# Optimization experiments

Measured on AMD Instinct MI355X. Metric: run time of the kernel, lower is better.

## Reference

```python
import jax, jax.numpy as jnp
import numpy as np

B, S, L, E, H, T, V, D = 32, 256, 24, 300, 256, 16, 50000, 256  # batch, sents, words/sent, emb, gru_units, topics, vocab, dense


def setup_inputs() -> dict:
    key = jax.random.key(0)
    ks = jax.random.split(key, 12)
    word_ids = jax.random.randint(ks[0], (B, S, L), 0, V, dtype=jnp.int32)
    tsize = S // T
    starts = (jnp.arange(T, dtype=jnp.int32) * tsize + 1)          # 1-indexed inclusive
    ends = (jnp.arange(T, dtype=jnp.int32) * tsize + tsize)
    topic_start_ends = jnp.broadcast_to(jnp.stack([starts, ends], -1)[None], (B, T, 2))
    g = lambda k, shape, sc=0.05: (jax.random.normal(k, shape, jnp.float32) * sc)
    return {
        "word_ids": word_ids,
        "topic_start_ends": topic_start_ends,
        "emb": g(ks[1], (V, E), 0.1),
        "Wih_f": g(ks[2], (3 * H, E)), "Whh_f": g(ks[3], (3 * H, H)),
        "bih_f": jnp.zeros((3 * H,), jnp.float32), "bhh_f": jnp.zeros((3 * H,), jnp.float32),
        "Wih_b": g(ks[4], (3 * H, E)), "Whh_b": g(ks[5], (3 * H, H)),
        "bih_b": jnp.zeros((3 * H,), jnp.float32), "bhh_b": jnp.zeros((3 * H,), jnp.float32),
        "W_att": g(ks[6], (4 * H, 4 * H)), "v_att": g(ks[7], (4 * H, 1)),
        "W_dna": g(ks[8], (4 * H, D)), "b_dna": jnp.zeros((D,), jnp.float32),
        "W_out": g(ks[9], (D, 1)), "b_out": jnp.zeros((1,), jnp.float32),
    }


def _gru_dir(x, Wih, Whh, bih, bhh, reverse):
    # x: [B, S, E] -> outputs [B, S, H], final hidden [B, H]  (PyTorch GRU cell math)
    def step(h, xt):
        gi = xt @ Wih.T + bih
        gh = h @ Whh.T + bhh
        ir, iz, inn = jnp.split(gi, 3, axis=-1)
        hr, hz, hn = jnp.split(gh, 3, axis=-1)
        r = jax.nn.sigmoid(ir + hr)
        z = jax.nn.sigmoid(iz + hz)
        n = jnp.tanh(inn + r * hn)
        h2 = (1.0 - z) * n + z * h
        return h2, h2
    h0 = jnp.zeros((x.shape[0], Whh.shape[1]), x.dtype)
    hT, ys = jax.lax.scan(step, h0, jnp.swapaxes(x, 0, 1), reverse=reverse)
    return jnp.swapaxes(ys, 0, 1), hT


def _gather_seq(x, idx):
    # x: [B, S', C], idx: [B, K] -> [B, K, C]
    return jnp.take_along_axis(x, idx[:, :, None].astype(jnp.int32), axis=1)


def reference(word_ids, topic_start_ends, emb, Wih_f, Whh_f, bih_f, bhh_f,
              Wih_b, Whh_b, bih_b, bhh_b, W_att, v_att, W_dna, b_dna, W_out, b_out):
    # --- sent_encoder: per-sentence mean of word embeddings ---
    sent_vecs = jnp.mean(emb[word_ids], axis=2)  # [B, S, E]

    # --- doc_encoder: bidirectional GRU ---
    out_f, hT_f = _gru_dir(sent_vecs, Wih_f, Whh_f, bih_f, bhh_f, reverse=False)
    out_b, hT_b = _gru_dir(sent_vecs, Wih_b, Whh_b, bih_b, bhh_b, reverse=True)
    sent_rep = jnp.concatenate([out_f, out_b], axis=-1)          # [B, S, 2H]
    hidden = jnp.stack([hT_f, hT_b], axis=0)                     # [2, B, H]
    # faithful to torch: hidden.view(batch_size, 2H) (row-major reshape)
    doc_vec = hidden.reshape(B, 2 * H)
    doc_rep = jnp.broadcast_to(doc_vec[:, None, :], (B, S, 2 * H))

    # --- topic representation via boundary differencing on front/back-padded output ---
    padded = jnp.pad(sent_rep, ((0, 0), (1, 1), (0, 0)))         # [B, S+2, 2H]
    starts = topic_start_ends[..., 0]                            # [B, T], 1-indexed
    ends = topic_start_ends[..., 1]
    topic_fwd = _gather_seq(padded, ends)[..., :H] - _gather_seq(padded, starts - 1)[..., :H]
    topic_bwd = _gather_seq(padded, starts)[..., H:] - _gather_seq(padded, ends + 1)[..., H:]
    topic_mat = jnp.concatenate([topic_fwd, topic_bwd], axis=-1)  # [B, T, 2H]
    # sentence s (0-indexed) -> topic t with starts[t] <= s+1 <= ends[t]
    sent_1idx = jnp.arange(1, S + 1, dtype=jnp.int32)
    topic_id = jax.vmap(lambda e: jnp.searchsorted(e, sent_1idx, side='left'))(ends)  # [B, S]
    topic_rep = jnp.take_along_axis(topic_mat, topic_id[:, :, None], axis=1)          # [B, S, 2H]

    # --- decoder_attention ---
    cat_ds = jnp.concatenate([doc_rep, sent_rep], axis=-1)       # [B, S, 4H]
    cat_ts = jnp.concatenate([topic_rep, sent_rep], axis=-1)
    doc_scores = jnp.tanh(cat_ds @ W_att) @ v_att                # [B, S, 1]
    topic_scores = jnp.tanh(cat_ts @ W_att) @ v_att
    doc_w = jax.nn.softmax(doc_scores, axis=1)
    topic_w = jax.nn.softmax(topic_scores, axis=1)
    context = doc_w * doc_rep + topic_w * topic_rep              # [B, S, 2H]
    inp = jnp.concatenate([sent_rep, context], axis=-1)          # [B, S, 4H]
    h = jax.nn.relu(inp @ W_dna + b_dna)                         # dropout is identity (eval)
    logits = (h @ W_out + b_out)[..., 0]                         # [B, S]
    return logits
```

## Files before the change

kernel.cpp:

```cpp
#include <hip/hip_runtime.h>
#include <hip/hip_bf16.h>
#include <math.h>

#define Bd 32
#define Sd 256
#define Ld 24
#define Ed 300
#define Hd 256
#define Td 16
#define Dd 256
#define EP 320
#define HPAD 264

using short8 = __attribute__((ext_vector_type(8))) short;
using f32x4  = __attribute__((ext_vector_type(4))) float;

__device__ __forceinline__ float fsigm(float x) { return 1.f / (1.f + __expf(-x)); }
__device__ __forceinline__ float ftanh(float x) {
  float e = __expf(2.f * x);
  return 1.f - 2.f / (e + 1.f);
}

__global__ void sent_means_kernel(const int* __restrict__ wids,
                                  const float* __restrict__ emb,
                                  __hip_bfloat16* __restrict__ apad) {
  int r = blockIdx.x;
  __shared__ int ids[Ld];
  int tid = threadIdx.x;
  if (tid < Ld) ids[tid] = wids[r * Ld + tid];
  __syncthreads();
  float acc = 0.f;
  if (tid < Ed) {
#pragma unroll
    for (int w = 0; w < Ld; ++w) acc += emb[(size_t)ids[w] * Ed + tid];
    acc *= (1.f / 24.f);
  }
  apad[r * EP + tid] = __float2bfloat16(tid < Ed ? acc : 0.f);
}

__global__ void pad_wih_kernel(const float* __restrict__ src,
                               __hip_bfloat16* __restrict__ dst) {
  int i = blockIdx.x * 256 + threadIdx.x;
  if (i >= 768 * EP) return;
  int n = i / EP, k = i % EP;
  dst[i] = __float2bfloat16(k < Ed ? src[n * Ed + k] : 0.f);
}
__global__ void f2bf_kernel(const float* __restrict__ src,
                            __hip_bfloat16* __restrict__ dst, int n) {
  int i = blockIdx.x * 256 + threadIdx.x;
  if (i < n) dst[i] = __float2bfloat16(src[i]);
}
__global__ void transpose_att_kernel(const float* __restrict__ src,
                                     __hip_bfloat16* __restrict__ dst) {
  int i = blockIdx.x * 256 + threadIdx.x;
  int n = i >> 10, k = i & 1023;
  dst[i] = __float2bfloat16(src[k * 1024 + n]);
}
__global__ void transpose_dna_kernel(const float* __restrict__ src,
                                     __hip_bfloat16* __restrict__ dst) {
  int i = blockIdx.x * 256 + threadIdx.x;
  int n = i >> 10, k = i & 1023;
  dst[i] = __float2bfloat16(src[k * Dd + n]);
}

__global__ __launch_bounds__(256) void gemm_xwt_kernel(
    const __hip_bfloat16* __restrict__ A, int lda,
    const __hip_bfloat16* __restrict__ W, int ldw,
    float* __restrict__ C, int ldc,
    int M, int N, int K,
    const float* __restrict__ bias) {
  __shared__ unsigned short la[64][32];
  __shared__ unsigned short lb[64][32];
  const int tid = threadIdx.x;
  const int m0 = blockIdx.x * 64, n0 = blockIdx.y * 64;
  const int lane = tid & 63, wid = tid >> 6;
  const int wm = (wid >> 1) * 32, wn = (wid & 1) * 32;
  const int lrow = tid >> 2, lcol = (tid & 3) * 8;
  f32x4 acc00 = {0.f, 0.f, 0.f, 0.f}, acc01 = {0.f, 0.f, 0.f, 0.f};
  f32x4 acc10 = {0.f, 0.f, 0.f, 0.f}, acc11 = {0.f, 0.f, 0.f, 0.f};
  int arow = m0 + lrow; if (arow > M - 1) arow = M - 1;
  const int brow = n0 + lrow;
  const int fr = lane & 15, fq = (lane >> 4) * 8;
  for (int k0 = 0; k0 < K; k0 += 32) {
    uint4 av = *(const uint4*)(A + (size_t)arow * lda + k0 + lcol);
    uint4 bv = *(const uint4*)(W + (size_t)brow * ldw + k0 + lcol);
    *(uint4*)(&la[lrow][lcol]) = av;
    *(uint4*)(&lb[lrow][lcol]) = bv;
    __syncthreads();
    short8 a0 = *(const short8*)(&la[wm + fr][fq]);
    short8 a1 = *(const short8*)(&la[wm + 16 + fr][fq]);
    short8 b0 = *(const short8*)(&lb[wn + fr][fq]);
    short8 b1 = *(const short8*)(&lb[wn + 16 + fr][fq]);
    acc00 = __builtin_amdgcn_mfma_f32_16x16x32_bf16(a0, b0, acc00, 0, 0, 0);
    acc01 = __builtin_amdgcn_mfma_f32_16x16x32_bf16(a0, b1, acc01, 0, 0, 0);
    acc10 = __builtin_amdgcn_mfma_f32_16x16x32_bf16(a1, b0, acc10, 0, 0, 0);
    acc11 = __builtin_amdgcn_mfma_f32_16x16x32_bf16(a1, b1, acc11, 0, 0, 0);
    __syncthreads();
  }
  const int rq = (lane >> 4) * 4;
  f32x4 accs[2][2] = {{acc00, acc01}, {acc10, acc11}};
  for (int i = 0; i < 2; ++i)
    for (int j = 0; j < 2; ++j) {
      int n = n0 + wn + j * 16 + fr;
      float bv = bias ? bias[n] : 0.f;
      for (int r2 = 0; r2 < 4; ++r2) {
        int m = m0 + wm + i * 16 + rq + r2;
        if (m < M) C[(size_t)m * ldc + n] = accs[i][j][r2] + bv;
      }
    }
}

__global__ __launch_bounds__(512, 2) void gru_mfma_kernel(
    const float* __restrict__ gi_f, const float* __restrict__ gi_b,
    const __hip_bfloat16* __restrict__ whhbf_f, const __hip_bfloat16* __restrict__ whhbf_b,
    const float* __restrict__ bhh_f, const float* __restrict__ bhh_b,
    float* __restrict__ sent_rep, __hip_bfloat16* __restrict__ sent_rep_bf,
    float* __restrict__ hT_f, float* __restrict__ hT_b) {
  __shared__ __hip_bfloat16 h_bf[16 * HPAD];
  __shared__ float h32[256];
  __shared__ float gh[768];
  __shared__ float stg32[8][256];
  __shared__ __hip_bfloat16 stgbf[8][256];
  const int blk = blockIdx.x;
  const int dir = blk >> 5, b = blk & 31;
  const int tid = threadIdx.x;
  const int lane = tid & 63, w = tid >> 6;
  const float* gi = dir ? gi_b : gi_f;
  const __hip_bfloat16* whh = dir ? whhbf_b : whhbf_f;
  const float* bhh = dir ? bhh_b : bhh_f;

  for (int i = tid; i < 16 * HPAD; i += 512) h_bf[i] = __float2bfloat16(0.f);
  if (tid < 256) h32[tid] = 0.f;

  short8 bfrag[6][8];
  {
    const int n0 = w * 96 + (lane & 15);
    const int kq = (lane >> 4) * 8;
#pragma unroll
    for (int nt = 0; nt < 6; ++nt)
#pragma unroll
      for (int kt = 0; kt < 8; ++kt)
        bfrag[nt][kt] = *(const short8*)(whh + (size_t)(n0 + nt * 16) * 256 + kt * 32 + kq);
  }
  float bhr = 0.f, bhz = 0.f, bhn = 0.f;
  if (tid < 256) { bhr = bhh[tid]; bhz = bhh[256 + tid]; bhn = bhh[512 + tid]; }
  __syncthreads();

  const int arow = (lane & 15) * HPAD;
  const int akq = (lane >> 4) * 8;

  for (int t = 0; t < Sd; ++t) {
    const int s = dir ? (Sd - 1 - t) : t;
    const size_t row = (size_t)((b << 8) + s);
    float gir = 0.f, giz = 0.f, gin = 0.f;
    if (tid < 256) {
      gir = gi[row * 768 + tid];
      giz = gi[row * 768 + 256 + tid];
      gin = gi[row * 768 + 512 + tid];
    }
    f32x4 acc[6];
#pragma unroll
    for (int nt = 0; nt < 6; ++nt) acc[nt] = (f32x4){0.f, 0.f, 0.f, 0.f};
    short8 a_cur = *(const short8*)(&h_bf[arow + akq]);
#pragma unroll
    for (int kt = 0; kt < 8; ++kt) {
      short8 a_nxt = a_cur;
      if (kt < 7) a_nxt = *(const short8*)(&h_bf[arow + (kt + 1) * 32 + akq]);
#pragma unroll
      for (int nt = 0; nt < 6; ++nt)
        acc[nt] = __builtin_amdgcn_mfma_f32_16x16x32_bf16(a_cur, bfrag[nt][kt], acc[nt], 0, 0, 0);
      a_cur = a_nxt;
    }
    if (lane < 16) {
#pragma unroll
      for (int nt = 0; nt < 6; ++nt)
        gh[w * 96 + nt * 16 + lane] = acc[nt][0];
    }
    __syncthreads();
    if (tid < 256) {
      float r = fsigm(gir + gh[tid] + bhr);
      float z = fsigm(giz + gh[256 + tid] + bhz);
      float n = ftanh(gin + r * (gh[512 + tid] + bhn));
      float hn = (1.f - z) * n + z * h32[tid];
      h32[tid] = hn;
      h_bf[tid] = __float2bfloat16(hn);
      stg32[t & 7][tid] = hn;
      stgbf[t & 7][tid] = __float2bfloat16(hn);
    }
    __syncthreads();
    if ((t & 7) == 7) {
      const int base = t - 7;
#pragma unroll
      for (int i = 0; i < 4; ++i) {
        int idx = tid + i * 512;
        int u = idx >> 8, d = idx & 255;
        int sg = dir ? (255 - (base + u)) : (base + u);
        size_t rowg = (size_t)((b << 8) + sg);
        int col = dir ? (256 + d) : d;
        sent_rep[rowg * 512 + col] = stg32[u][d];
        sent_rep_bf[rowg * 512 + col] = stgbf[u][d];
      }
    }
  }
  if (tid < 256) (dir ? hT_b : hT_f)[b * 256 + tid] = h32[tid];
}

__global__ void docvec_kernel(const float* __restrict__ hTf, const float* __restrict__ hTb,
                              __hip_bfloat16* __restrict__ dv) {
  int b = blockIdx.x, jj = threadIdx.x;
  int idx = b * 512 + jj;
  int dsel = idx >> 13;
  int rem = idx & 8191;
  int bp = rem >> 8, hp = rem & 255;
  float v = (dsel ? hTb : hTf)[bp * Hd + hp];
  dv[idx] = __float2bfloat16(v);
}

__global__ void topic_kernel(const int* __restrict__ tse, const float* __restrict__ sent_rep,
                             __hip_bfloat16* __restrict__ topic_bf) {
  int bt = blockIdx.x;
  int b = bt >> 4;
  int st = tse[bt * 2], en = tse[bt * 2 + 1];
  int dd = threadIdx.x;
  auto pad = [&](int i, int col) -> float {
    if (i < 1 || i > Sd) return 0.f;
    return sent_rep[((size_t)((b << 8) + (i - 1))) * 512 + col];
  };
  float fwd = pad(en, dd) - pad(st - 1, dd);
  float bwd = pad(st, Hd + dd) - pad(en + 1, Hd + dd);
  topic_bf[(size_t)bt * 512 + dd] = __float2bfloat16(fwd);
  topic_bf[(size_t)bt * 512 + Hd + dd] = __float2bfloat16(bwd);
}

__global__ void scores_kernel(const float* __restrict__ P, const float* __restrict__ R,
                              const float* __restrict__ Q, const float* __restrict__ v_att,
                              const int* __restrict__ tse,
                              float* __restrict__ dsc, float* __restrict__ tsc) {
  int r = blockIdx.x;
  int b = r >> 8, s = r & 255;
  int tid = threadIdx.x;
  int tsel = Td - 1;
  for (int t = 0; t < Td; ++t) {
    if (tse[(b * Td + t) * 2 + 1] >= s + 1) { tsel = t; break; }
  }
  const float* q = Q + (size_t)r * 1024;
  const float* p = P + (size_t)b * 1024;
  const float* rr = R + (size_t)(b * Td + tsel) * 1024;
  float accd = 0.f, acct = 0.f;
  for (int n = tid; n < 1024; n += 256) {
    float qv = q[n];
    float vv = v_att[n];
    accd += ftanh(p[n] + qv) * vv;
    acct += ftanh(rr[n] + qv) * vv;
  }
  __shared__ float s1[256], s2[256];
  s1[tid] = accd; s2[tid] = acct;
  __syncthreads();
  for (int off = 128; off > 0; off >>= 1) {
    if (tid < off) { s1[tid] += s1[tid + off]; s2[tid] += s2[tid + off]; }
    __syncthreads();
  }
  if (tid == 0) { dsc[r] = s1[0]; tsc[r] = s2[0]; }
}

__global__ void softmax_kernel(const float* __restrict__ dsc, const float* __restrict__ tsc,
                               float* __restrict__ dw, float* __restrict__ tw) {
  int b = blockIdx.x, s = threadIdx.x;
  __shared__ float red[256];
  for (int which = 0; which < 2; ++which) {
    const float* src = which ? tsc : dsc;
    float v = src[b * Sd + s];
    red[s] = v; __syncthreads();
    for (int off = 128; off > 0; off >>= 1) {
      if (s < off) red[s] = fmaxf(red[s], red[s + off]);
      __syncthreads();
    }
    float m = red[0]; __syncthreads();
    float e = __expf(v - m);
    red[s] = e; __syncthreads();
    for (int off = 128; off > 0; off >>= 1) {
      if (s < off) red[s] += red[s + off];
      __syncthreads();
    }
    float sum = red[0]; __syncthreads();
    (which ? tw : dw)[b * Sd + s] = e / sum;
  }
}

__global__ void final_kernel(const float* __restrict__ U, const float* __restrict__ dvd,
                             const float* __restrict__ tvd, const float* __restrict__ dw,
                             const float* __restrict__ tw, const float* __restrict__ b_dna,
                             const float* __restrict__ w_out,
                             const float* __restrict__ b_out,
                             const int* __restrict__ tse, float* __restrict__ out) {
  int r = blockIdx.x;
  int b = r >> 8, s = r & 255;
  int dd = threadIdx.x;
  int tsel = Td - 1;
  for (int t = 0; t < Td; ++t) {
    if (tse[(b * Td + t) * 2 + 1] >= s + 1) { tsel = t; break; }
  }
  float wdv = dw[b * Sd + s], wtv = tw[b * Sd + s];
  float x = U[(size_t)r * Dd + dd] + wdv * dvd[b * Dd + dd] +
            wtv * tvd[(size_t)(b * Td + tsel) * Dd + dd] + b_dna[dd];
  x = fmaxf(x, 0.f);
  float term = x * w_out[dd];
  __shared__ float red[256];
  red[dd] = term; __syncthreads();
  for (int off = 128; off > 0; off >>= 1) {
    if (dd < off) red[dd] += red[dd + off];
    __syncthreads();
  }
  if (dd == 0) out[r] = red[0] + b_out[0];
}

static void launch_gemm(const __hip_bfloat16* A, int lda, const __hip_bfloat16* W, int ldw,
                        float* C, int ldc, int M, int N, int K,
                        const float* bias, hipStream_t stream) {
  dim3 grid((M + 63) / 64, N / 64);
  gemm_xwt_kernel<<<grid, 256, 0, stream>>>(A, lda, W, ldw, C, ldc, M, N, K, bias);
}

extern "C" void kernel_launch(void* const* d_in, const int* in_sizes, int n_in,
                              void* d_out, int out_size, void* d_ws, size_t ws_size,
                              hipStream_t stream) {
  const int* word_ids = (const int*)d_in[0];
  const int* tse      = (const int*)d_in[1];
  const float* emb   = (const float*)d_in[2];
  const float* wih_f = (const float*)d_in[3];
  const float* whh_f = (const float*)d_in[4];
  const float* bih_f = (const float*)d_in[5];
  const float* bhh_f = (const float*)d_in[6];
  const float* wih_b = (const float*)d_in[7];
  const float* whh_b = (const float*)d_in[8];
  const float* bih_b = (const float*)d_in[9];
  const float* bhh_b = (const float*)d_in[10];
  const float* w_att = (const float*)d_in[11];
  const float* v_att = (const float*)d_in[12];
  const float* w_dna = (const float*)d_in[13];
  const float* b_dna = (const float*)d_in[14];
  const float* w_out = (const float*)d_in[15];
  const float* b_out = (const float*)d_in[16];
  float* out = (float*)d_out;
  char* ws = (char*)d_ws;

  const int M = Bd * Sd;

  size_t off = 0;
  auto alloc = [&](size_t sz) { size_t o = off; off += (sz + 255) & ~(size_t)255; return o; };
  size_t o_svbf   = alloc((size_t)M * EP * 2);
  size_t o_wpadf  = alloc((size_t)768 * EP * 2);
  size_t o_wpadb  = alloc((size_t)768 * EP * 2);
  size_t o_whhbf  = alloc((size_t)768 * Hd * 2 * 2);
  size_t o_wattT  = alloc((size_t)1024 * 1024 * 2);
  size_t o_wdnaT  = alloc((size_t)Dd * 1024 * 2);
  size_t o_hTf    = alloc((size_t)Bd * Hd * 4);
  size_t o_hTb    = alloc((size_t)Bd * Hd * 4);
  size_t o_dvbf   = alloc((size_t)Bd * 512 * 2);
  size_t o_topbf  = alloc((size_t)Bd * Td * 512 * 2);
  size_t o_P      = alloc((size_t)Bd * 1024 * 4);
  size_t o_R      = alloc((size_t)Bd * Td * 1024 * 4);
  size_t o_dvd    = alloc((size_t)Bd * Dd * 4);
  size_t o_tvd    = alloc((size_t)Bd * Td * Dd * 4);
  size_t o_dsc    = alloc((size_t)Bd * Sd * 4);
  size_t o_tsc    = alloc((size_t)Bd * Sd * 4);
  size_t o_dw     = alloc((size_t)Bd * Sd * 4);
  size_t o_tw     = alloc((size_t)Bd * Sd * 4);
  size_t o_srep32 = alloc((size_t)M * 512 * 4);
  size_t o_srepbf = alloc((size_t)M * 512 * 2);
  size_t o_gif    = alloc((size_t)M * 768 * 4);
  size_t o_gib    = alloc((size_t)M * 768 * 4);
  size_t o_Q = o_gif;
  size_t o_U = o_gif + (size_t)M * 1024 * 4;
  (void)ws_size;

  __hip_bfloat16* svbf   = (__hip_bfloat16*)(ws + o_svbf);
  __hip_bfloat16* wpadf  = (__hip_bfloat16*)(ws + o_wpadf);
  __hip_bfloat16* wpadb  = (__hip_bfloat16*)(ws + o_wpadb);
  __hip_bfloat16* whhbf_f = (__hip_bfloat16*)(ws + o_whhbf);
  __hip_bfloat16* whhbf_b = whhbf_f + 768 * Hd;
  __hip_bfloat16* wattT  = (__hip_bfloat16*)(ws + o_wattT);
  __hip_bfloat16* wdnaT  = (__hip_bfloat16*)(ws + o_wdnaT);
  float* hTf = (float*)(ws + o_hTf);
  float* hTb = (float*)(ws + o_hTb);
  __hip_bfloat16* dvbf  = (__hip_bfloat16*)(ws + o_dvbf);
  __hip_bfloat16* topbf = (__hip_bfloat16*)(ws + o_topbf);
  float* P   = (float*)(ws + o_P);
  float* R   = (float*)(ws + o_R);
  float* dvd = (float*)(ws + o_dvd);
  float* tvd = (float*)(ws + o_tvd);
  float* dsc = (float*)(ws + o_dsc);
  float* tsc = (float*)(ws + o_tsc);
  float* dw  = (float*)(ws + o_dw);
  float* tw  = (float*)(ws + o_tw);
  float* srep32 = (float*)(ws + o_srep32);
  __hip_bfloat16* srepbf = (__hip_bfloat16*)(ws + o_srepbf);
  float* gif = (float*)(ws + o_gif);
  float* gib = (float*)(ws + o_gib);
  float* Q = (float*)(ws + o_Q);
  float* U = (float*)(ws + o_U);

  sent_means_kernel<<<M, EP, 0, stream>>>(word_ids, emb, svbf);
  pad_wih_kernel<<<(768 * EP) / 256, 256, 0, stream>>>(wih_f, wpadf);
  pad_wih_kernel<<<(768 * EP) / 256, 256, 0, stream>>>(wih_b, wpadb);
  f2bf_kernel<<<(768 * Hd) / 256, 256, 0, stream>>>(whh_f, whhbf_f, 768 * Hd);
  f2bf_kernel<<<(768 * Hd) / 256, 256, 0, stream>>>(whh_b, whhbf_b, 768 * Hd);
  transpose_att_kernel<<<(1024 * 1024) / 256, 256, 0, stream>>>(w_att, wattT);
  transpose_dna_kernel<<<(Dd * 1024) / 256, 256, 0, stream>>>(w_dna, wdnaT);
  launch_gemm(svbf, EP, wpadf, EP, gif, 768, M, 768, EP, bih_f, stream);
  launch_gemm(svbf, EP, wpadb, EP, gib, 768, M, 768, EP, bih_b, stream);
  gru_mfma_kernel<<<64, 512, 0, stream>>>(gif, gib, whhbf_f, whhbf_b, bhh_f, bhh_b,
                                          srep32, srepbf, hTf, hTb);
  docvec_kernel<<<Bd, 512, 0, stream>>>(hTf, hTb, dvbf);
  topic_kernel<<<Bd * Td, 256, 0, stream>>>(tse, srep32, topbf);
  launch_gemm(srepbf, 512, wattT + 512, 1024, Q, 1024, M, 1024, 512, nullptr, stream);
  launch_gemm(dvbf, 512, wattT, 1024, P, 1024, Bd, 1024, 512, nullptr, stream);
  launch_gemm(topbf, 512, wattT, 1024, R, 1024, Bd * Td, 1024, 512, nullptr, stream);
  launch_gemm(srepbf, 512, wdnaT, 1024, U, Dd, M, Dd, 512, nullptr, stream);
  launch_gemm(dvbf, 512, wdnaT + 512, 1024, dvd, Dd, Bd, Dd, 512, nullptr, stream);
  launch_gemm(topbf, 512, wdnaT + 512, 1024, tvd, Dd, Bd * Td, Dd, 512, nullptr, stream);
  scores_kernel<<<M, 256, 0, stream>>>(P, R, Q, v_att, tse, dsc, tsc);
  softmax_kernel<<<Bd, 256, 0, stream>>>(dsc, tsc, dw, tw);
  final_kernel<<<M, 256, 0, stream>>>(U, dvd, tvd, dw, tw, b_dna, w_out, b_out, tse, out);
}
```

Baseline: 616.1 us.

## Fuse GRU gate math into MFMA lanes with double-buffered hidden state

Remaps the recurrent weight fragments so each wave computes the r, z and n gate columns for the same 32 hidden units. The gate nonlinearities can then be evaluated directly from the MFMA accumulators, with no shared gh buffer and one barrier per timestep instead of two. The hidden tile is double-buffered, staging is widened to 16 rows to avoid write-after-read hazards, and the input-gate projections are prefetched two steps ahead in registers. The risk is that only 16 lanes per wave do the gate math, and the hand-written waitcnt/barrier must correctly order the LDS writes.

```diff
diff --git a/kernel.cpp b/kernel.cpp
--- a/kernel.cpp
+++ b/kernel.cpp
@@ -116,11 +116,9 @@
     const float* __restrict__ bhh_f, const float* __restrict__ bhh_b,
     float* __restrict__ sent_rep, __hip_bfloat16* __restrict__ sent_rep_bf,
     float* __restrict__ hT_f, float* __restrict__ hT_b) {
-  __shared__ __hip_bfloat16 h_bf[16 * HPAD];
-  __shared__ float h32[256];
-  __shared__ float gh[768];
-  __shared__ float stg32[8][256];
-  __shared__ __hip_bfloat16 stgbf[8][256];
+  __shared__ __hip_bfloat16 htile[2][16 * HPAD];
+  __shared__ float stg32[16][256];
+  __shared__ __hip_bfloat16 stgbf[16][256];
   const int blk = blockIdx.x;
   const int dir = blk >> 5, b = blk & 31;
   const int tid = threadIdx.x;
@@ -129,80 +127,107 @@
   const __hip_bfloat16* whh = dir ? whhbf_b : whhbf_f;
   const float* bhh = dir ? bhh_b : bhh_f;
 
-  for (int i = tid; i < 16 * HPAD; i += 512) h_bf[i] = __float2bfloat16(0.f);
-  if (tid < 256) h32[tid] = 0.f;
+  for (int i = tid; i < 16 * HPAD; i += 512) {
+    htile[0][i] = __float2bfloat16(0.f);
+    htile[1][i] = __float2bfloat16(0.f);
+  }
+
+  const int c = lane & 15;
+  const int kq = (lane >> 4) * 8;
+  const int d0 = w * 32 + c, d1 = d0 + 16;
 
   short8 bfrag[6][8];
-  {
-    const int n0 = w * 96 + (lane & 15);
-    const int kq = (lane >> 4) * 8;
-#pragma unroll
-    for (int nt = 0; nt < 6; ++nt)
+#pragma unroll
+  for (int g = 0; g < 3; ++g)
+#pragma unroll
+    for (int a = 0; a < 2; ++a)
 #pragma unroll
       for (int kt = 0; kt < 8; ++kt)
-        bfrag[nt][kt] = *(const short8*)(whh + (size_t)(n0 + nt * 16) * 256 + kt * 32 + kq);
-  }
-  float bhr = 0.f, bhz = 0.f, bhn = 0.f;
-  if (tid < 256) { bhr = bhh[tid]; bhz = bhh[256 + tid]; bhn = bhh[512 + tid]; }
-  __syncthreads();
-
-  const int arow = (lane & 15) * HPAD;
-  const int akq = (lane >> 4) * 8;
-
-  for (int t = 0; t < Sd; ++t) {
-    const int s = dir ? (Sd - 1 - t) : t;
-    const size_t row = (size_t)((b << 8) + s);
-    float gir = 0.f, giz = 0.f, gin = 0.f;
-    if (tid < 256) {
-      gir = gi[row * 768 + tid];
-      giz = gi[row * 768 + 256 + tid];
-      gin = gi[row * 768 + 512 + tid];
-    }
+        bfrag[g * 2 + a][kt] =
+            *(const short8*)(whh + (size_t)(g * 256 + w * 32 + a * 16 + c) * 256 + kt * 32 + kq);
+
+  float bh[3][2] = {{0.f, 0.f}, {0.f, 0.f}, {0.f, 0.f}};
+  float hreg[2] = {0.f, 0.f};
+  float gA[3][2], gB[3][2];
+  if (lane < 16) {
+#pragma unroll
+    for (int g = 0; g < 3; ++g) {
+      bh[g][0] = bhh[g * 256 + d0];
+      bh[g][1] = bhh[g * 256 + d1];
+    }
+    const size_t r0 = (size_t)((b << 8) + (dir ? 255 : 0));
+    const size_t r1 = (size_t)((b << 8) + (dir ? 254 : 1));
+#pragma unroll
+    for (int g = 0; g < 3; ++g) {
+      gA[g][0] = gi[r0 * 768 + g * 256 + d0];
+      gA[g][1] = gi[r0 * 768 + g * 256 + d1];
+      gB[g][0] = gi[r1 * 768 + g * 256 + d0];
+      gB[g][1] = gi[r1 * 768 + g * 256 + d1];
+    }
+  }
+  asm volatile("s_waitcnt lgkmcnt(0)\n\ts_barrier" ::: "memory");
+
+  auto body = [&](int t, float (&gc)[3][2]) {
+    const __hip_bfloat16* hsrc = htile[t & 1];
+    __hip_bfloat16* hdst = htile[(t + 1) & 1];
     f32x4 acc[6];
 #pragma unroll
     for (int nt = 0; nt < 6; ++nt) acc[nt] = (f32x4){0.f, 0.f, 0.f, 0.f};
-    short8 a_cur = *(const short8*)(&h_bf[arow + akq]);
 #pragma unroll
     for (int kt = 0; kt < 8; ++kt) {
-      short8 a_nxt = a_cur;
-      if (kt < 7) a_nxt = *(const short8*)(&h_bf[arow + (kt + 1) * 32 + akq]);
+      short8 av = *(const short8*)(&hsrc[c * HPAD + kt * 32 + kq]);
 #pragma unroll
       for (int nt = 0; nt < 6; ++nt)
-        acc[nt] = __builtin_amdgcn_mfma_f32_16x16x32_bf16(a_cur, bfrag[nt][kt], acc[nt], 0, 0, 0);
-      a_cur = a_nxt;
+        acc[nt] = __builtin_amdgcn_mfma_f32_16x16x32_bf16(av, bfrag[nt][kt], acc[nt], 0, 0, 0);
     }
     if (lane < 16) {
 #pragma unroll
-      for (int nt = 0; nt < 6; ++nt)
-        gh[w * 96 + nt * 16 + lane] = acc[nt][0];
-    }
-    __syncthreads();
-    if (tid < 256) {
-      float r = fsigm(gir + gh[tid] + bhr);
-      float z = fsigm(giz + gh[256 + tid] + bhz);
-      float n = ftanh(gin + r * (gh[512 + tid] + bhn));
-      float hn = (1.f - z) * n + z * h32[tid];
-      h32[tid] = hn;
-      h_bf[tid] = __float2bfloat16(hn);
-      stg32[t & 7][tid] = hn;
-      stgbf[t & 7][tid] = __float2bfloat16(hn);
-    }
-    __syncthreads();
+      for (int a = 0; a < 2; ++a) {
+        int d = a ? d1 : d0;
+        float rr = fsigm(gc[0][a] + acc[a][0] + bh[0][a]);
+        float zz = fsigm(gc[1][a] + acc[2 + a][0] + bh[1][a]);
+        float nn = ftanh(gc[2][a] + rr * (acc[4 + a][0] + bh[2][a]));
+        float hn = (1.f - zz) * nn + zz * hreg[a];
+        hreg[a] = hn;
+        hdst[d] = __float2bfloat16(hn);
+        stg32[t & 15][d] = hn;
+        stgbf[t & 15][d] = __float2bfloat16(hn);
+      }
+      if (t + 2 < Sd) {
+        const size_t row2 = (size_t)((b << 8) + (dir ? (255 - (t + 2)) : (t + 2)));
+#pragma unroll
+        for (int g = 0; g < 3; ++g) {
+          gc[g][0] = gi[row2 * 768 + g * 256 + d0];
+          gc[g][1] = gi[row2 * 768 + g * 256 + d1];
+        }
+      }
+    }
+    asm volatile("s_waitcnt lgkmcnt(0)\n\ts_barrier" ::: "memory");
     if ((t & 7) == 7) {
       const int base = t - 7;
 #pragma unroll
       for (int i = 0; i < 4; ++i) {
         int idx = tid + i * 512;
         int u = idx >> 8, d = idx & 255;
-        int sg = dir ? (255 - (base + u)) : (base + u);
+        int st_ = base + u;
+        int sg = dir ? (255 - st_) : st_;
         size_t rowg = (size_t)((b << 8) + sg);
         int col = dir ? (256 + d) : d;
-        sent_rep[rowg * 512 + col] = stg32[u][d];
-        sent_rep_bf[rowg * 512 + col] = stgbf[u][d];
+        sent_rep[rowg * 512 + col] = stg32[st_ & 15][d];
+        sent_rep_bf[rowg * 512 + col] = stgbf[st_ & 15][d];
       }
     }
-  }
-  if (tid < 256) (dir ? hT_b : hT_f)[b * 256 + tid] = h32[tid];
+  };
+
+  for (int t = 0; t < Sd; t += 2) {
+    body(t, gA);
+    body(t + 1, gB);
+  }
+  if (lane < 16) {
+    float* hT = dir ? hT_b : hT_f;
+    hT[b * 256 + d0] = hreg[0];
+    hT[b * 256 + d1] = hreg[1];
+  }
 }
 
 __global__ void docvec_kernel(const float* __restrict__ hTf, const float* __restrict__ hTb,
```

New measurement: 964.3 us. 56.5% more time.

## Prefetch GRU input gates into double-buffered LDS and shrink hidden-state buffer

Applied to the files above, without the earlier changes.

The GRU recurrence kernel now loads the precomputed input-gate rows for eight timesteps at a time into a double-buffered LDS area, issuing the next burst eight steps ahead. This replaces three dependent global loads per step on the serial critical path. The padded 16-row bf16 A-operand buffer becomes a single 256-element row, with lanes other than row 0 feeding zeros to the MFMA. The fp32 hidden state is kept in a register, and the bf16 staging copy is dropped in favour of converting at writeback. The larger LDS footprint (about 49KB for gi buffers) may reduce occupancy, and the prefetch still stalls on global latency because the loads are synchronous.

```diff
diff --git a/kernel.cpp b/kernel.cpp
--- a/kernel.cpp
+++ b/kernel.cpp
@@ -10,7 +10,6 @@
 #define Td 16
 #define Dd 256
 #define EP 320
-#define HPAD 264
 
 using short8 = __attribute__((ext_vector_type(8))) short;
 using f32x4  = __attribute__((ext_vector_type(4))) float;
@@ -116,11 +115,10 @@
     const float* __restrict__ bhh_f, const float* __restrict__ bhh_b,
     float* __restrict__ sent_rep, __hip_bfloat16* __restrict__ sent_rep_bf,
     float* __restrict__ hT_f, float* __restrict__ hT_b) {
-  __shared__ __hip_bfloat16 h_bf[16 * HPAD];
-  __shared__ float h32[256];
+  __shared__ float gi_lds[2][8][768];
+  __shared__ __hip_bfloat16 h_bf[256];
   __shared__ float gh[768];
   __shared__ float stg32[8][256];
-  __shared__ __hip_bfloat16 stgbf[8][256];
   const int blk = blockIdx.x;
   const int dir = blk >> 5, b = blk & 31;
   const int tid = threadIdx.x;
@@ -129,8 +127,7 @@
   const __hip_bfloat16* whh = dir ? whhbf_b : whhbf_f;
   const float* bhh = dir ? bhh_b : bhh_f;
 
-  for (int i = tid; i < 16 * HPAD; i += 512) h_bf[i] = __float2bfloat16(0.f);
-  if (tid < 256) h32[tid] = 0.f;
+  if (tid < 256) h_bf[tid] = __float2bfloat16(0.f);
 
   short8 bfrag[6][8];
   {
@@ -142,34 +139,39 @@
       for (int kt = 0; kt < 8; ++kt)
         bfrag[nt][kt] = *(const short8*)(whh + (size_t)(n0 + nt * 16) * 256 + kt * 32 + kq);
   }
-  float bhr = 0.f, bhz = 0.f, bhn = 0.f;
+  float bhr = 0.f, bhz = 0.f, bhn = 0.f, hprev = 0.f;
   if (tid < 256) { bhr = bhh[tid]; bhz = bhh[256 + tid]; bhn = bhh[512 + tid]; }
+
+  auto burst = [&](int tstart, int buf) {
+#pragma unroll
+    for (int i = 0; i < 3; ++i) {
+      int idx = tid + i * 512;
+      int u = idx / 192;
+      int c4 = (idx - u * 192) * 4;
+      int s = dir ? (255 - (tstart + u)) : (tstart + u);
+      float4 v = *(const float4*)(gi + (size_t)(((b << 8) + s) * 768 + c4));
+      *(float4*)(&gi_lds[buf][u][c4]) = v;
+    }
+  };
+  burst(0, 0);
   __syncthreads();
 
-  const int arow = (lane & 15) * HPAD;
-  const int akq = (lane >> 4) * 8;
+  const int c = lane & 15;
+  const int kq = (lane >> 4) * 8;
+  const short8 zero8 = {0, 0, 0, 0, 0, 0, 0, 0};
 
   for (int t = 0; t < Sd; ++t) {
-    const int s = dir ? (Sd - 1 - t) : t;
-    const size_t row = (size_t)((b << 8) + s);
-    float gir = 0.f, giz = 0.f, gin = 0.f;
-    if (tid < 256) {
-      gir = gi[row * 768 + tid];
-      giz = gi[row * 768 + 256 + tid];
-      gin = gi[row * 768 + 512 + tid];
-    }
+    if ((t & 7) == 0 && t + 8 < Sd) burst(t + 8, ((t >> 3) + 1) & 1);
     f32x4 acc[6];
 #pragma unroll
     for (int nt = 0; nt < 6; ++nt) acc[nt] = (f32x4){0.f, 0.f, 0.f, 0.f};
-    short8 a_cur = *(const short8*)(&h_bf[arow + akq]);
 #pragma unroll
     for (int kt = 0; kt < 8; ++kt) {
-      short8 a_nxt = a_cur;
-      if (kt < 7) a_nxt = *(const short8*)(&h_bf[arow + (kt + 1) * 32 + akq]);
+      short8 av = *(const short8*)(&h_bf[kt * 32 + kq]);
+      if (c != 0) av = zero8;
 #pragma unroll
       for (int nt = 0; nt < 6; ++nt)
-        acc[nt] = __builtin_amdgcn_mfma_f32_16x16x32_bf16(a_cur, bfrag[nt][kt], acc[nt], 0, 0, 0);
-      a_cur = a_nxt;
+        acc[nt] = __builtin_amdgcn_mfma_f32_16x16x32_bf16(av, bfrag[nt][kt], acc[nt], 0, 0, 0);
     }
     if (lane < 16) {
 #pragma unroll
@@ -178,14 +180,14 @@
     }
     __syncthreads();
     if (tid < 256) {
-      float r = fsigm(gir + gh[tid] + bhr);
-      float z = fsigm(giz + gh[256 + tid] + bhz);
-      float n = ftanh(gin + r * (gh[512 + tid] + bhn));
-      float hn = (1.f - z) * n + z * h32[tid];
-      h32[tid] = hn;
+      const float* gl = gi_lds[(t >> 3) & 1][t & 7];
+      float rr = fsigm(gl[tid] + gh[tid] + bhr);
+      float zz = fsigm(gl[256 + tid] + gh[256 + tid] + bhz);
+      float nn = ftanh(gl[512 + tid] + rr * (gh[512 + tid] + bhn));
+      float hn = (1.f - zz) * nn + zz * hprev;
+      hprev = hn;
       h_bf[tid] = __float2bfloat16(hn);
       stg32[t & 7][tid] = hn;
-      stgbf[t & 7][tid] = __float2bfloat16(hn);
     }
     __syncthreads();
     if ((t & 7) == 7) {
@@ -197,12 +199,13 @@
         int sg = dir ? (255 - (base + u)) : (base + u);
         size_t rowg = (size_t)((b << 8) + sg);
         int col = dir ? (256 + d) : d;
-        sent_rep[rowg * 512 + col] = stg32[u][d];
-        sent_rep_bf[rowg * 512 + col] = stgbf[u][d];
+        float v = stg32[u][d];
+        sent_rep[rowg * 512 + col] = v;
+        sent_rep_bf[rowg * 512 + col] = __float2bfloat16(v);
       }
     }
   }
-  if (tid < 256) (dir ? hT_b : hT_f)[b * 256 + tid] = h32[tid];
+  if (tid < 256) (dir ? hT_b : hT_f)[b * 256 + tid] = hprev;
 }
 
 __global__ void docvec_kernel(const float* __restrict__ hTf, const float* __restrict__ hTb,
```

After: 623.3 us. Within noise of the previous version (+1.2%).
